# Kernel tuning notes

Measured on AMD Instinct MI355X. Metric: run time of the kernel, lower is better.

Reference implementation:

```python
import jax, jax.numpy as jnp
import numpy as np

B, T, D, H = 8, 2048, 1024, 16
HD = D // H          # head_dim = 64
SC = H               # scales = n_heads = 16
DECAY_MIN, DECAY_MAX = 0.3, 0.99


def setup_inputs() -> dict:
    key = jax.random.key(0)
    k_x, k_in, k_mix, k_gw, k_gb, k_out = jax.random.split(key, 6)
    x = jax.random.normal(k_x, (B, T, D), dtype=jnp.float32)
    pad_mask = jnp.zeros((B, T), dtype=bool)  # True = PAD
    inv = 1.0 / np.sqrt(D)
    W_in = jax.random.uniform(k_in, (D, D), jnp.float32, -inv, inv)
    W_out = jax.random.uniform(k_out, (D, D), jnp.float32, -inv, inv)
    W_gate = jax.random.uniform(k_gw, (D, D), jnp.float32, -inv, inv)
    b_gate = jax.random.uniform(k_gb, (D,), jnp.float32, -inv, inv)
    state_mix = jax.random.normal(k_mix, (H, SC, HD), jnp.float32) / np.sqrt(HD)
    p = jnp.linspace(DECAY_MIN, DECAY_MAX, SC)
    logit_decay = jnp.tile(jnp.log(p / (1.0 - p))[None, :], (H, 1))  # [H, SC]
    return {"x": x, "pad_mask": pad_mask, "W_in": W_in, "state_mix": state_mix,
            "logit_decay": logit_decay, "W_gate": W_gate, "b_gate": b_gate,
            "W_out": W_out}


def reference(x, pad_mask, W_in, state_mix, logit_decay, W_gate, b_gate, W_out):
    Bc, Tc, Dc = x.shape
    Hc, Sc, Hd = state_mix.shape
    h = (x @ W_in.T).reshape(Bc, Tc, Hc, Hd)          # [B,T,H,Hd]
    decays = jax.nn.sigmoid(logit_decay)              # [H,SC]
    keep = 1.0 - pad_mask.astype(x.dtype)             # [B,T], 1 where not PAD

    def step(S, inp):
        ht, mt = inp                                  # [B,H,Hd], [B]
        S = (decays[None, :, :, None] * S + ht[:, :, None, :]) \
            * mt[:, None, None, None]                 # [B,H,SC,Hd]
        read = jnp.einsum('bhsd,hsd->bhd', S, state_mix)
        return S, read

    S0 = jnp.zeros((Bc, Hc, Sc, Hd), dtype=x.dtype)
    _, reads = jax.lax.scan(step, S0, (h.transpose(1, 0, 2, 3), keep.T))
    y = reads.transpose(1, 0, 2, 3).reshape(Bc, Tc, Dc)
    g = jax.nn.sigmoid(x @ W_gate.T + b_gate)
    y = g * y + (1.0 - g) * x
    return y @ W_out.T
```

## Files before the change

kernel.cpp:

```cpp
#include <hip/hip_runtime.h>

#define B_  8
#define T_  2048
#define D_  1024
#define H_  16
#define HD_ 64
#define SC_ 16
#define NC_ 32
#define CT_ 64

typedef __attribute__((ext_vector_type(8))) short short8;
typedef __attribute__((ext_vector_type(4))) float f32x4;

__device__ inline unsigned short f2bf(float f) {
  union { float f; unsigned u; } v; v.f = f;
  unsigned r = v.u + 0x7FFFu + ((v.u >> 16) & 1u);
  return (unsigned short)(r >> 16);
}
__device__ inline float bf2f(unsigned short b) {
  union { unsigned u; float f; } v; v.u = ((unsigned)b) << 16; return v.f;
}

__device__ inline void gl_lds16(const unsigned short* g, unsigned short* l) {
  __builtin_amdgcn_global_load_lds(
      (const __attribute__((address_space(1))) unsigned int*)(g),
      (__attribute__((address_space(3))) unsigned int*)(l), 16, 0, 0);
}

__global__ void conv_f32_bf16(const float* __restrict__ in,
                              unsigned short* __restrict__ out, int n4) {
  int i = blockIdx.x * 256 + threadIdx.x;
  if (i >= n4) return;
  float4 v = ((const float4*)in)[i];
  ushort4 o;
  o.x = f2bf(v.x); o.y = f2bf(v.y); o.z = f2bf(v.z); o.w = f2bf(v.w);
  ((ushort4*)out)[i] = o;
}

template<int MODE>
__global__ __launch_bounds__(512, 1)
void gemm256(const unsigned short* __restrict__ A,
             const unsigned short* __restrict__ Bt,
             void* __restrict__ C1, void* __restrict__ C2,
             const float* __restrict__ bgate,
             int M, int N, int K) {
  __shared__ unsigned short lds[3 * 16384];
  const int tid  = threadIdx.x;
  const int lane = tid & 63;
  const int w    = tid >> 6;
  const int wm   = w >> 2, wn = w & 3;
  const int l15  = lane & 15, l4 = lane >> 4;
  const int srow = lane >> 2;
  const int gc   = (lane & 3) ^ ((lane >> 3) & 3);
  const int aslot = l4 ^ ((l15 >> 1) & 3);

  const int nbn = N >> 8;
  const int nwg = gridDim.x;
  int bid = blockIdx.x;
  int b2 = (bid & 7) * (nwg >> 3) + (bid >> 3);
  const int bm = (b2 / nbn) << 8;
  const int bn = (b2 % nbn) << 8;

  const unsigned short* Ag0 = A  + (size_t)(bm + (w * 2 + 0) * 16 + srow) * K + gc * 8;
  const unsigned short* Ag1 = A  + (size_t)(bm + (w * 2 + 1) * 16 + srow) * K + gc * 8;
  const unsigned short* Bg0 = Bt + (size_t)(bn + (w * 2 + 0) * 16 + srow) * K + gc * 8;
  const unsigned short* Bg1 = Bt + (size_t)(bn + (w * 2 + 1) * 16 + srow) * K + gc * 8;

#define STAGE_A(t, buf) do {                                      \
    size_t _g = (size_t)(t) * 32;                                 \
    gl_lds16(Ag0 + _g, &lds[(buf) * 16384 + (w * 2 + 0) * 512]);  \
    gl_lds16(Ag1 + _g, &lds[(buf) * 16384 + (w * 2 + 1) * 512]);  \
  } while (0)
#define STAGE_B(t, buf) do {                                      \
    size_t _g = (size_t)(t) * 32;                                 \
    gl_lds16(Bg0 + _g, &lds[(buf) * 16384 + 8192 + (w * 2 + 0) * 512]); \
    gl_lds16(Bg1 + _g, &lds[(buf) * 16384 + 8192 + (w * 2 + 1) * 512]); \
  } while (0)

  f32x4 acc[8][4] = {};
  const int nt = K >> 5;

  STAGE_A(0, 0); STAGE_B(0, 0);
  STAGE_A(1, 1); STAGE_B(1, 1);
  asm volatile("s_waitcnt vmcnt(4)" ::: "memory");
  asm volatile("s_barrier" ::: "memory");

  int bufc = 0;
  int bufs = 2;
  for (int t = 0; t < nt; ++t) {
    const unsigned short* Ab = &lds[bufc * 16384];
    const unsigned short* Bb = Ab + 8192;
    const bool do_stage = (t + 2 < nt);
    short8 afr[4], bfr[4];

    if (do_stage) STAGE_A(t + 2, bufs);
#pragma unroll
    for (int ni = 0; ni < 4; ++ni)
      bfr[ni] = *(const short8*)(Bb + (wn * 64 + ni * 16 + l15) * 32 + aslot * 8);
#pragma unroll
    for (int mi = 0; mi < 4; ++mi)
      afr[mi] = *(const short8*)(Ab + (wm * 128 + mi * 16 + l15) * 32 + aslot * 8);
    __builtin_amdgcn_s_setprio(1);
#pragma unroll
    for (int mi = 0; mi < 4; ++mi)
#pragma unroll
      for (int ni = 0; ni < 4; ++ni)
        acc[mi][ni] = __builtin_amdgcn_mfma_f32_16x16x32_bf16(
            afr[mi], bfr[ni], acc[mi][ni], 0, 0, 0);
    __builtin_amdgcn_s_setprio(0);

    if (do_stage) STAGE_B(t + 2, bufs);
#pragma unroll
    for (int mi = 0; mi < 4; ++mi)
      afr[mi] = *(const short8*)(Ab + (wm * 128 + (mi + 4) * 16 + l15) * 32 + aslot * 8);
    __builtin_amdgcn_s_setprio(1);
#pragma unroll
    for (int mi = 0; mi < 4; ++mi)
#pragma unroll
      for (int ni = 0; ni < 4; ++ni)
        acc[mi + 4][ni] = __builtin_amdgcn_mfma_f32_16x16x32_bf16(
            afr[mi], bfr[ni], acc[mi + 4][ni], 0, 0, 0);
    __builtin_amdgcn_s_setprio(0);

    if (t < nt - 2)
      asm volatile("s_waitcnt vmcnt(4)" ::: "memory");
    else if (t == nt - 2)
      asm volatile("s_waitcnt vmcnt(0)" ::: "memory");
    asm volatile("s_barrier" ::: "memory");
    bufc = (bufc == 2) ? 0 : bufc + 1;
    bufs = (bufs == 2) ? 0 : bufs + 1;
  }
#undef STAGE_A
#undef STAGE_B

  const int rbase = bm + wm * 128 + (l4 << 2);
  const bool is_gate = (MODE == 2) && (bn >= 1024);
  void* dst = is_gate ? C2 : C1;
  const int cb = is_gate ? (bn - 1024) : bn;
  const int cbase = cb + wn * 64 + l15;
  const int CN = (MODE == 2) ? 1024 : N;
  float bgv[4];
  if (is_gate) {
#pragma unroll
    for (int ni = 0; ni < 4; ++ni) bgv[ni] = bgate[cbase + (ni << 4)];
  }
#pragma unroll
  for (int mi = 0; mi < 8; ++mi)
#pragma unroll
    for (int ni = 0; ni < 4; ++ni)
#pragma unroll
      for (int r = 0; r < 4; ++r) {
        size_t row = rbase + (mi << 4) + r;
        int col = cbase + (ni << 4);
        if (MODE == 0) {
          ((float*)dst)[row * CN + col] = acc[mi][ni][r];
        } else if (is_gate) {
          float g = 1.f / (1.f + __expf(-(acc[mi][ni][r] + bgv[ni])));
          ((unsigned short*)dst)[row * CN + col] = f2bf(g);
        } else {
          ((unsigned short*)dst)[row * CN + col] = f2bf(acc[mi][ni][r]);
        }
      }
}

__device__ inline bool chunk_has_pad(const unsigned char* pp) {
  const unsigned long long* p8 = (const unsigned long long*)pp;
  unsigned long long v = 0;
#pragma unroll
  for (int i = 0; i < CT_ / 8; ++i) v |= p8[i];
  return v != 0ull;
}

__global__ void scan_pass1(const unsigned short* __restrict__ hb,
                           const unsigned char* __restrict__ pad,
                           const float* __restrict__ ldec,
                           float* __restrict__ Schunk,
                           float* __restrict__ akeep) {
  int gid = blockIdx.x * 256 + threadIdx.x;
  int d  = gid & 63;
  int hh = (gid >> 6) & 15;
  int c  = (gid >> 10) & (NC_ - 1);
  int b  = gid >> 15;
  float dec[SC_], S[SC_];
#pragma unroll
  for (int s = 0; s < SC_; ++s) {
    dec[s] = 1.f / (1.f + __expf(-ldec[hh * SC_ + s]));
    S[s] = 0.f;
  }
  const int t0 = c * CT_;
  const unsigned short* hp = hb + (size_t)(b * T_ + t0) * D_ + hh * HD_ + d;
  const unsigned char* pp = pad + b * T_ + t0;
  bool anypad = chunk_has_pad(pp);
  if (!anypad) {
    for (int t = 0; t < CT_; ++t) {
      float ht = bf2f(*hp); hp += D_;
#pragma unroll
      for (int s = 0; s < SC_; ++s) S[s] = dec[s] * S[s] + ht;
    }
  } else {
    for (int t = 0; t < CT_; ++t) {
      float ht = bf2f(*hp); hp += D_;
      float k = pp[t] ? 0.f : 1.f;
#pragma unroll
      for (int s = 0; s < SC_; ++s) S[s] = (dec[s] * S[s] + ht) * k;
    }
  }
  size_t base = ((size_t)((b * NC_ + c) * H_ + hh) * SC_) * HD_ + d;
#pragma unroll
  for (int s = 0; s < SC_; ++s) Schunk[base + s * HD_] = S[s];
  if (hh == 0 && d == 0) akeep[b * NC_ + c] = anypad ? 0.f : 1.f;
}

__global__ void scan_combine(float* __restrict__ Schunk,
                             const float* __restrict__ akeep,
                             const float* __restrict__ ldec) {
  int gid = blockIdx.x * 256 + threadIdx.x;
  int d  = gid & 63;
  int s  = (gid >> 6) & 15;
  int hh = (gid >> 10) & 15;
  int b  = gid >> 14;
  float dec  = 1.f / (1.f + __expf(-ldec[hh * SC_ + s]));
  float dpow = __powf(dec, (float)CT_);
  float carry = 0.f;
  for (int c = 0; c < NC_; ++c) {
    size_t idx = ((size_t)((b * NC_ + c) * H_ + hh) * SC_ + s) * HD_ + d;
    float e = Schunk[idx];
    Schunk[idx] = carry;
    float Ac = (akeep[b * NC_ + c] != 0.f) ? dpow : 0.f;
    carry = Ac * carry + e;
  }
}

__global__ void scan_pass2(const unsigned short* __restrict__ hb,
                           const unsigned char* __restrict__ pad,
                           const float* __restrict__ ldec,
                           const float* __restrict__ mix,
                           const float* __restrict__ Sstart,
                           const unsigned short* __restrict__ gb,
                           unsigned short* __restrict__ xy) {
  int gid = blockIdx.x * 256 + threadIdx.x;
  int d  = gid & 63;
  int hh = (gid >> 6) & 15;
  int c  = (gid >> 10) & (NC_ - 1);
  int b  = gid >> 15;
  float dec[SC_], mx[SC_], S[SC_];
  size_t sbase = ((size_t)((b * NC_ + c) * H_ + hh) * SC_) * HD_ + d;
#pragma unroll
  for (int s = 0; s < SC_; ++s) {
    dec[s] = 1.f / (1.f + __expf(-ldec[hh * SC_ + s]));
    mx[s]  = mix[(hh * SC_ + s) * HD_ + d];
    S[s]   = Sstart[sbase + s * HD_];
  }
  const int t0 = c * CT_;
  const int col = hh * HD_ + d;
  size_t off = (size_t)(b * T_ + t0) * D_ + col;
  const unsigned char* pp = pad + b * T_ + t0;
  bool anypad = chunk_has_pad(pp);
  if (!anypad) {
    for (int t = 0; t < CT_; ++t, off += D_) {
      float ht = bf2f(hb[off]);
      float rd = 0.f;
#pragma unroll
      for (int s = 0; s < SC_; ++s) {
        S[s] = dec[s] * S[s] + ht;
        rd  += mx[s] * S[s];
      }
      float g  = bf2f(gb[off]);
      float xv = bf2f(xy[off]);
      xy[off] = f2bf(fmaf(g, rd - xv, xv));
    }
  } else {
    for (int t = 0; t < CT_; ++t, off += D_) {
      float ht = bf2f(hb[off]);
      float k = pp[t] ? 0.f : 1.f;
      float rd = 0.f;
#pragma unroll
      for (int s = 0; s < SC_; ++s) {
        S[s] = (dec[s] * S[s] + ht) * k;
        rd  += mx[s] * S[s];
      }
      float g  = bf2f(gb[off]);
      float xv = bf2f(xy[off]);
      xy[off] = f2bf(fmaf(g, rd - xv, xv));
    }
  }
}

extern "C" void kernel_launch(void* const* d_in, const int* in_sizes, int n_in,
                              void* d_out, int out_size, void* d_ws, size_t ws_size,
                              hipStream_t stream) {
  const float* x          = (const float*)d_in[0];
  const unsigned char* pm = (const unsigned char*)d_in[1];
  const float* W_in       = (const float*)d_in[2];
  const float* smix       = (const float*)d_in[3];
  const float* ldec       = (const float*)d_in[4];
  const float* W_gate     = (const float*)d_in[5];
  const float* b_gate     = (const float*)d_in[6];
  const float* W_out      = (const float*)d_in[7];
  float* out = (float*)d_out;
  char* ws = (char*)d_ws;

  const int NX = B_ * T_ * D_;
  const int NW = D_ * D_;

  unsigned short* xb    = (unsigned short*)(ws);
  unsigned short* wbin  = (unsigned short*)(ws + 33554432);
  unsigned short* wbgt  = (unsigned short*)(ws + 35651584);
  unsigned short* wbout = (unsigned short*)(ws + 37748736);
  unsigned short* hb    = (unsigned short*)(ws + 39845888);
  float* Schunk         = (float*)(ws + 73400320);
  float* akeep          = (float*)(ws + 90177536);
  unsigned short* gb    = (unsigned short*)d_out;

  conv_f32_bf16<<<NX / 1024, 256, 0, stream>>>(x, xb, NX / 4);
  conv_f32_bf16<<<NW / 1024, 256, 0, stream>>>(W_in,   wbin,  NW / 4);
  conv_f32_bf16<<<NW / 1024, 256, 0, stream>>>(W_gate, wbgt,  NW / 4);
  conv_f32_bf16<<<NW / 1024, 256, 0, stream>>>(W_out,  wbout, NW / 4);

  const int M = B_ * T_;

  dim3 gg2((M / 256) * (2048 / 256));
  gemm256<2><<<gg2, 512, 0, stream>>>(xb, wbin, hb, gb, b_gate, M, 2048, D_);

  dim3 sg1(B_ * NC_ * H_ * HD_ / 256);
  dim3 sgc(B_ * H_ * SC_ * HD_ / 256);
  scan_pass1 <<<sg1, 256, 0, stream>>>(hb, pm, ldec, Schunk, akeep);
  scan_combine<<<sgc, 256, 0, stream>>>(Schunk, akeep, ldec);
  scan_pass2 <<<sg1, 256, 0, stream>>>(hb, pm, ldec, smix, Schunk, gb, xb);

  dim3 gg((M / 256) * (D_ / 256));
  gemm256<0><<<gg, 512, 0, stream>>>(xb, wbout, out, nullptr, nullptr, M, D_, D_);
}
```

Measured before the change: 228.4 us.

## Deepen GEMM pipeline to four LDS stages, halve scan chunks, merge weight conversions

The GEMM moves from three to four LDS buffers with a prefetch distance of three and adds extra barriers around the staging loads. The scan uses 64 chunks of 32 steps instead of 32 chunks of 64, which shortens each thread's serial scan but doubles the per-chunk state written and combined. Chunk states now live in the spare second half of the output buffer. Pass2's read reduction is split into four independent accumulators to shorten the dependency chain. The three weight conversions are merged into a single launch.

```diff
diff --git a/kernel.cpp b/kernel.cpp
--- a/kernel.cpp
+++ b/kernel.cpp
@@ -6,8 +6,8 @@
 #define H_  16
 #define HD_ 64
 #define SC_ 16
-#define NC_ 32
-#define CT_ 64
+#define NC_ 64
+#define CT_ 32
 
 typedef __attribute__((ext_vector_type(8))) short short8;
 typedef __attribute__((ext_vector_type(4))) float f32x4;
@@ -37,6 +37,21 @@
   ((ushort4*)out)[i] = o;
 }
 
+__global__ void conv_w3(const float* __restrict__ w0, unsigned short* __restrict__ o0,
+                        const float* __restrict__ w1, unsigned short* __restrict__ o1,
+                        const float* __restrict__ w2, unsigned short* __restrict__ o2) {
+  int bid = blockIdx.x;
+  const float* in; unsigned short* out;
+  if (bid < 1024)      { in = w0; out = o0; }
+  else if (bid < 2048) { in = w1; out = o1; bid -= 1024; }
+  else                 { in = w2; out = o2; bid -= 2048; }
+  int i = bid * 256 + threadIdx.x;
+  float4 v = ((const float4*)in)[i];
+  ushort4 o;
+  o.x = f2bf(v.x); o.y = f2bf(v.y); o.z = f2bf(v.z); o.w = f2bf(v.w);
+  ((ushort4*)out)[i] = o;
+}
+
 template<int MODE>
 __global__ __launch_bounds__(512, 1)
 void gemm256(const unsigned short* __restrict__ A,
@@ -44,7 +59,7 @@
              void* __restrict__ C1, void* __restrict__ C2,
              const float* __restrict__ bgate,
              int M, int N, int K) {
-  __shared__ unsigned short lds[3 * 16384];
+  __shared__ unsigned short lds[4 * 16384];
   const int tid  = threadIdx.x;
   const int lane = tid & 63;
   const int w    = tid >> 6;
@@ -66,40 +81,40 @@
   const unsigned short* Bg0 = Bt + (size_t)(bn + (w * 2 + 0) * 16 + srow) * K + gc * 8;
   const unsigned short* Bg1 = Bt + (size_t)(bn + (w * 2 + 1) * 16 + srow) * K + gc * 8;
 
-#define STAGE_A(t, buf) do {                                      \
-    size_t _g = (size_t)(t) * 32;                                 \
-    gl_lds16(Ag0 + _g, &lds[(buf) * 16384 + (w * 2 + 0) * 512]);  \
-    gl_lds16(Ag1 + _g, &lds[(buf) * 16384 + (w * 2 + 1) * 512]);  \
+#define STAGE_A(kof, buf) do {                                          \
+    gl_lds16(Ag0 + (kof), &lds[(buf) * 16384 + (w * 2 + 0) * 512]);     \
+    gl_lds16(Ag1 + (kof), &lds[(buf) * 16384 + (w * 2 + 1) * 512]);     \
   } while (0)
-#define STAGE_B(t, buf) do {                                      \
-    size_t _g = (size_t)(t) * 32;                                 \
-    gl_lds16(Bg0 + _g, &lds[(buf) * 16384 + 8192 + (w * 2 + 0) * 512]); \
-    gl_lds16(Bg1 + _g, &lds[(buf) * 16384 + 8192 + (w * 2 + 1) * 512]); \
+#define STAGE_B(kof, buf) do {                                          \
+    gl_lds16(Bg0 + (kof), &lds[(buf) * 16384 + 8192 + (w * 2 + 0) * 512]); \
+    gl_lds16(Bg1 + (kof), &lds[(buf) * 16384 + 8192 + (w * 2 + 1) * 512]); \
   } while (0)
 
   f32x4 acc[8][4] = {};
   const int nt = K >> 5;
 
-  STAGE_A(0, 0); STAGE_B(0, 0);
-  STAGE_A(1, 1); STAGE_B(1, 1);
-  asm volatile("s_waitcnt vmcnt(4)" ::: "memory");
+  STAGE_A(0, 0);  STAGE_B(0, 0);
+  STAGE_A(32, 1); STAGE_B(32, 1);
+  STAGE_A(64, 2); STAGE_B(64, 2);
+  asm volatile("s_waitcnt vmcnt(8)" ::: "memory");
   asm volatile("s_barrier" ::: "memory");
 
-  int bufc = 0;
-  int bufs = 2;
-  for (int t = 0; t < nt; ++t) {
-    const unsigned short* Ab = &lds[bufc * 16384];
+  for (int kt = 0; kt < nt; ++kt) {
+    const unsigned short* Ab = &lds[(kt & 3) * 16384];
     const unsigned short* Bb = Ab + 8192;
-    const bool do_stage = (t + 2 < nt);
+    const bool st = (kt + 3 < nt);
+    const int sbuf = (kt + 3) & 3;
+    const size_t skof = (size_t)(kt + 3) * 32;
     short8 afr[4], bfr[4];
 
-    if (do_stage) STAGE_A(t + 2, bufs);
 #pragma unroll
     for (int ni = 0; ni < 4; ++ni)
       bfr[ni] = *(const short8*)(Bb + (wn * 64 + ni * 16 + l15) * 32 + aslot * 8);
 #pragma unroll
     for (int mi = 0; mi < 4; ++mi)
       afr[mi] = *(const short8*)(Ab + (wm * 128 + mi * 16 + l15) * 32 + aslot * 8);
+    if (st) STAGE_A(skof, sbuf);
+    asm volatile("s_barrier" ::: "memory");
     __builtin_amdgcn_s_setprio(1);
 #pragma unroll
     for (int mi = 0; mi < 4; ++mi)
@@ -108,11 +123,13 @@
         acc[mi][ni] = __builtin_amdgcn_mfma_f32_16x16x32_bf16(
             afr[mi], bfr[ni], acc[mi][ni], 0, 0, 0);
     __builtin_amdgcn_s_setprio(0);
-
-    if (do_stage) STAGE_B(t + 2, bufs);
+    asm volatile("s_barrier" ::: "memory");
+
 #pragma unroll
     for (int mi = 0; mi < 4; ++mi)
       afr[mi] = *(const short8*)(Ab + (wm * 128 + (mi + 4) * 16 + l15) * 32 + aslot * 8);
+    if (st) STAGE_B(skof, sbuf);
+    asm volatile("s_barrier" ::: "memory");
     __builtin_amdgcn_s_setprio(1);
 #pragma unroll
     for (int mi = 0; mi < 4; ++mi)
@@ -122,13 +139,13 @@
             afr[mi], bfr[ni], acc[mi + 4][ni], 0, 0, 0);
     __builtin_amdgcn_s_setprio(0);
 
-    if (t < nt - 2)
+    if (kt <= nt - 4)
+      asm volatile("s_waitcnt vmcnt(8)" ::: "memory");
+    else if (kt == nt - 3)
       asm volatile("s_waitcnt vmcnt(4)" ::: "memory");
-    else if (t == nt - 2)
+    else if (kt == nt - 2)
       asm volatile("s_waitcnt vmcnt(0)" ::: "memory");
     asm volatile("s_barrier" ::: "memory");
-    bufc = (bufc == 2) ? 0 : bufc + 1;
-    bufs = (bufs == 2) ? 0 : bufs + 1;
   }
 #undef STAGE_A
 #undef STAGE_B
@@ -180,7 +197,7 @@
   int d  = gid & 63;
   int hh = (gid >> 6) & 15;
   int c  = (gid >> 10) & (NC_ - 1);
-  int b  = gid >> 15;
+  int b  = gid >> 16;
   float dec[SC_], S[SC_];
 #pragma unroll
   for (int s = 0; s < SC_; ++s) {
@@ -242,7 +259,7 @@
   int d  = gid & 63;
   int hh = (gid >> 6) & 15;
   int c  = (gid >> 10) & (NC_ - 1);
-  int b  = gid >> 15;
+  int b  = gid >> 16;
   float dec[SC_], mx[SC_], S[SC_];
   size_t sbase = ((size_t)((b * NC_ + c) * H_ + hh) * SC_) * HD_ + d;
 #pragma unroll
@@ -259,12 +276,15 @@
   if (!anypad) {
     for (int t = 0; t < CT_; ++t, off += D_) {
       float ht = bf2f(hb[off]);
-      float rd = 0.f;
-#pragma unroll
-      for (int s = 0; s < SC_; ++s) {
-        S[s] = dec[s] * S[s] + ht;
-        rd  += mx[s] * S[s];
+      float r0 = 0.f, r1 = 0.f, r2 = 0.f, r3 = 0.f;
+#pragma unroll
+      for (int j = 0; j < 4; ++j) {
+        S[j]      = dec[j]      * S[j]      + ht; r0 = fmaf(mx[j],      S[j],      r0);
+        S[j + 4]  = dec[j + 4]  * S[j + 4]  + ht; r1 = fmaf(mx[j + 4],  S[j + 4],  r1);
+        S[j + 8]  = dec[j + 8]  * S[j + 8]  + ht; r2 = fmaf(mx[j + 8],  S[j + 8],  r2);
+        S[j + 12] = dec[j + 12] * S[j + 12] + ht; r3 = fmaf(mx[j + 12], S[j + 12], r3);
       }
+      float rd = (r0 + r1) + (r2 + r3);
       float g  = bf2f(gb[off]);
       float xv = bf2f(xy[off]);
       xy[off] = f2bf(fmaf(g, rd - xv, xv));
@@ -273,12 +293,15 @@
     for (int t = 0; t < CT_; ++t, off += D_) {
       float ht = bf2f(hb[off]);
       float k = pp[t] ? 0.f : 1.f;
-      float rd = 0.f;
-#pragma unroll
-      for (int s = 0; s < SC_; ++s) {
-        S[s] = (dec[s] * S[s] + ht) * k;
-        rd  += mx[s] * S[s];
+      float r0 = 0.f, r1 = 0.f, r2 = 0.f, r3 = 0.f;
+#pragma unroll
+      for (int j = 0; j < 4; ++j) {
+        S[j]      = (dec[j]      * S[j]      + ht) * k; r0 = fmaf(mx[j],      S[j],      r0);
+        S[j + 4]  = (dec[j + 4]  * S[j + 4]  + ht) * k; r1 = fmaf(mx[j + 4],  S[j + 4],  r1);
+        S[j + 8]  = (dec[j + 8]  * S[j + 8]  + ht) * k; r2 = fmaf(mx[j + 8],  S[j + 8],  r2);
+        S[j + 12] = (dec[j + 12] * S[j + 12] + ht) * k; r3 = fmaf(mx[j + 12], S[j + 12], r3);
       }
+      float rd = (r0 + r1) + (r2 + r3);
       float g  = bf2f(gb[off]);
       float xv = bf2f(xy[off]);
       xy[off] = f2bf(fmaf(g, rd - xv, xv));
@@ -301,21 +324,18 @@
   char* ws = (char*)d_ws;
 
   const int NX = B_ * T_ * D_;
-  const int NW = D_ * D_;
 
   unsigned short* xb    = (unsigned short*)(ws);
   unsigned short* wbin  = (unsigned short*)(ws + 33554432);
   unsigned short* wbgt  = (unsigned short*)(ws + 35651584);
   unsigned short* wbout = (unsigned short*)(ws + 37748736);
   unsigned short* hb    = (unsigned short*)(ws + 39845888);
-  float* Schunk         = (float*)(ws + 73400320);
-  float* akeep          = (float*)(ws + 90177536);
+  float* akeep          = (float*)(ws + 73400320);
   unsigned short* gb    = (unsigned short*)d_out;
+  float* Schunk         = (float*)((char*)d_out + 33554432);
 
   conv_f32_bf16<<<NX / 1024, 256, 0, stream>>>(x, xb, NX / 4);
-  conv_f32_bf16<<<NW / 1024, 256, 0, stream>>>(W_in,   wbin,  NW / 4);
-  conv_f32_bf16<<<NW / 1024, 256, 0, stream>>>(W_gate, wbgt,  NW / 4);
-  conv_f32_bf16<<<NW / 1024, 256, 0, stream>>>(W_out,  wbout, NW / 4);
+  conv_w3<<<3072, 256, 0, stream>>>(W_in, wbin, W_gate, wbgt, W_out, wbout);
 
   const int M = B_ * T_;
 
```

Result: no change. 232.1 us (+1.6%).
